# Performance work log

Hardware: AMD Instinct MI355X
Metric: run time of the kernel (lower is better)

Reference implementation:

```python
import jax, jax.numpy as jnp
import numpy as np

D_MODEL = 1024
NUM_MODULES = 8
MAX_TRANSLATION = 3.0
MAX_ROT_ANGLE = 3.141592653589793


def setup_inputs() -> dict:
    key = jax.random.key(0)
    k1, k2, k3, k4 = jax.random.split(key, 4)
    B, N = 8, 8192
    node_feats = jax.random.normal(k1, (B, N, D_MODEL), jnp.float32)
    coords = jax.random.normal(k2, (B, N, 3), jnp.float32)
    W = jax.random.normal(k3, (NUM_MODULES * 8, D_MODEL), jnp.float32) * (1.0 / np.sqrt(D_MODEL))
    b = jax.random.normal(k4, (NUM_MODULES * 8,), jnp.float32) * 0.01
    return {"node_feats": node_feats, "coords": coords, "W": W, "b": b}


def _normalize(x, eps=1e-12):
    return x / jnp.clip(jnp.linalg.norm(x, axis=-1, keepdims=True), eps)


def _axis_angle_to_quaternion(aa):
    # pytorch3d convention: quat = [cos(theta/2), axis * sin(theta/2)]
    angles = jnp.linalg.norm(aa, axis=-1, keepdims=True)
    half = angles * 0.5
    small = jnp.abs(angles) < 1e-6
    safe_angles = jnp.where(small, 1.0, angles)
    sin_half_over_angle = jnp.where(small, 0.5 - angles * angles / 48.0, jnp.sin(half) / safe_angles)
    return jnp.concatenate([jnp.cos(half), aa * sin_half_over_angle], axis=-1)


def _quat_mul(a, b):
    aw, ax, ay, az = a[..., 0], a[..., 1], a[..., 2], a[..., 3]
    bw, bx, by, bz = b[..., 0], b[..., 1], b[..., 2], b[..., 3]
    ow = aw * bw - ax * bx - ay * by - az * bz
    ox = aw * bx + ax * bw + ay * bz - az * by
    oy = aw * by - ax * bz + ay * bw + az * bx
    oz = aw * bz + ax * by - ay * bx + az * bw
    return jnp.stack([ow, ox, oy, oz], axis=-1)


def _quat_apply(q, p):
    # q: [B,1,4], p: [B,N,3] -> rotate points: im(q * (0,p) * q^-1)
    pq = jnp.concatenate([jnp.zeros_like(p[..., :1]), p], axis=-1)
    q_inv = q * jnp.array([1.0, -1.0, -1.0, -1.0], q.dtype)
    return _quat_mul(_quat_mul(q, pq), q_inv)[..., 1:]


def reference(node_feats, coords, W, b):
    B, N, _ = coords.shape
    params = (node_feats @ W.T + b).reshape(B, N, NUM_MODULES, 8)
    anchor_logits = params[..., 0:1]   # [B,N,M,1]
    select_logits = params[..., 1:2]
    rot_axis = params[..., 2:5]
    trans = params[..., 5:8]

    anchor_w = jax.nn.softmax(anchor_logits, axis=1)      # softmax over N
    select_p = jax.nn.sigmoid(select_logits)

    angles = jnp.linalg.norm(rot_axis, axis=-1, keepdims=True)
    axis_n = _normalize(rot_axis)
    angles = jnp.tanh(angles) * MAX_ROT_ANGLE
    quats = _axis_angle_to_quaternion(axis_n * angles)    # [B,N,M,4]
    trans = jnp.tanh(trans) * MAX_TRANSLATION             # [B,N,M,3]

    xs = (jnp.moveaxis(quats, 2, 0),     # [M,B,N,4]
          jnp.moveaxis(trans, 2, 0),     # [M,B,N,3]
          jnp.moveaxis(anchor_w, 2, 0),  # [M,B,N,1]
          jnp.moveaxis(select_p, 2, 0))  # [M,B,N,1]

    def step(c, per):
        q, t, aw, sp = per
        anchor = jnp.sum(c * aw, axis=1, keepdims=True)               # [B,1,3]
        s = jnp.clip(jnp.sum(sp, axis=1, keepdims=True), 1e-8)        # [B,1,1]
        q_group = _normalize(jnp.sum(q * sp, axis=1, keepdims=True) / s)  # [B,1,4]
        t_group = jnp.sum(t * sp, axis=1, keepdims=True) / s          # [B,1,3]
        moved = _quat_apply(q_group, c - anchor) + anchor + t_group   # [B,N,3]
        return c + sp * (moved - c), None                             # lerp

    out, _ = jax.lax.scan(step, coords, xs)
    return out
```

## Files before the change

kernel.cpp:

```cpp
#include <hip/hip_runtime.h>
#include <hip/hip_bf16.h>
#include <math.h>

#define D_MODEL 1024
#define NMOD 8
#define BATCH 8
#define NNODE 8192
#define PI_F 3.14159265358979323846f
#define MAXT 3.0f

typedef short bf16x8 __attribute__((ext_vector_type(8)));
typedef float f32x4 __attribute__((ext_vector_type(4)));

__device__ inline unsigned short f2bf(float x) {
    __hip_bfloat16 h = __float2bfloat16(x);
    return __builtin_bit_cast(unsigned short, h);
}
__device__ inline float bf2f(unsigned short h) {
    unsigned u = ((unsigned)h) << 16;
    return __builtin_bit_cast(float, u);
}

__global__ void pack_b(const float* __restrict__ W, unsigned short* __restrict__ Bpk) {
    int t = blockIdx.x * 256 + threadIdx.x;
    int l  = t & 63;
    int g  = (t >> 6) & 3;
    int ks = t >> 8;
    int j  = g * 16 + (l & 15);
    int k0 = ks * 32 + ((l >> 4) * 8);
    const float* wp = &W[(size_t)j * D_MODEL + k0];
    bf16x8 pack;
    #pragma unroll
    for (int r = 0; r < 8; ++r) pack[r] = (short)f2bf(wp[r]);
    *reinterpret_cast<bf16x8*>(Bpk + (size_t)t * 8) = pack;
}

__global__ __launch_bounds__(256, 4) void gemm_mfma(
    const float* __restrict__ feats, const unsigned short* __restrict__ Bpk,
    const float* __restrict__ bias,
    float* __restrict__ ew_out, float* __restrict__ sp_out,
    float* __restrict__ sums)
{
    __shared__ float pbuf[4][16][68];
    __shared__ float sacc[64];

    const int tid  = threadIdx.x;
    const int lane = tid & 63;
    const int wv   = tid >> 6;

    if (tid < 64) sacc[tid] = 0.f;
    __syncthreads();

    const int mt    = blockIdx.x * 4 + wv;
    const int mbase = mt * 16;
    const float* arow = feats + (size_t)(mbase + (lane & 15)) * D_MODEL + ((lane >> 4) * 8);
    const bf16x8* bp = reinterpret_cast<const bf16x8*>(Bpk);

    f32x4 acc[4];
    #pragma unroll
    for (int g = 0; g < 4; ++g) acc[g] = (f32x4){0.f, 0.f, 0.f, 0.f};

    #pragma unroll 2
    for (int ks = 0; ks < 32; ++ks) {
        const float4 fa = *reinterpret_cast<const float4*>(arow + ks * 32);
        const float4 fb = *reinterpret_cast<const float4*>(arow + ks * 32 + 4);
        float f[8] = {fa.x, fa.y, fa.z, fa.w, fb.x, fb.y, fb.z, fb.w};
        bf16x8 ahi, alo;
        #pragma unroll
        for (int i = 0; i < 8; ++i) {
            unsigned short h = f2bf(f[i]);
            ahi[i] = (short)h;
            alo[i] = (short)f2bf(f[i] - bf2f(h));
        }
        #pragma unroll
        for (int g = 0; g < 4; ++g) {
            bf16x8 bh = bp[(ks * 4 + g) * 64 + lane];
            acc[g] = __builtin_amdgcn_mfma_f32_16x16x32_bf16(ahi, bh, acc[g], 0, 0, 0);
            acc[g] = __builtin_amdgcn_mfma_f32_16x16x32_bf16(alo, bh, acc[g], 0, 0, 0);
        }
    }

    #pragma unroll
    for (int g = 0; g < 4; ++g) {
        float bj = bias[g * 16 + (lane & 15)];
        #pragma unroll
        for (int r = 0; r < 4; ++r)
            pbuf[wv][(lane >> 4) * 4 + r][g * 16 + (lane & 15)] = acc[g][r] + bj;
    }

    const int b    = mbase >> 13;
    const int nInB = mbase & 8191;

    #pragma unroll
    for (int h = 0; h < 2; ++h) {
        const int node = lane & 15;
        const int m    = (lane >> 4) + 4 * h;
        const float* pa = &pbuf[wv][node][m * 8];
        float al = pa[0], sl = pa[1];
        float ax = pa[2], ay = pa[3], az = pa[4];
        float tx = pa[5], ty = pa[6], tz = pa[7];

        float ew = expf(al);
        float sp = 1.f / (1.f + expf(-sl));

        float n0  = sqrtf(ax * ax + ay * ay + az * az);
        float inv = 1.f / fmaxf(n0, 1e-12f);
        float ang = tanhf(n0) * PI_F;
        float hf  = 0.5f * ang;
        float shoa = (ang < 1e-6f) ? (0.5f - ang * ang * (1.f / 48.f))
                                   : (sinf(hf) / ang);
        float qw = cosf(hf);
        float fac = inv * ang * shoa;
        float qx = ax * fac, qy = ay * fac, qz = az * fac;

        float ttx = tanhf(tx) * MAXT, tty = tanhf(ty) * MAXT, ttz = tanhf(tz) * MAXT;

        size_t base = ((size_t)(b * NMOD + m)) * NNODE + nInB + node;
        ew_out[base] = ew;
        sp_out[base] = sp;

        float red[8];
        red[0] = sp;
        red[1] = sp * qw; red[2] = sp * qx; red[3] = sp * qy; red[4] = sp * qz;
        red[5] = sp * ttx; red[6] = sp * tty; red[7] = sp * ttz;
        #pragma unroll
        for (int v = 0; v < 8; ++v) {
            #pragma unroll
            for (int o = 1; o < 16; o <<= 1) red[v] += __shfl_xor(red[v], o);
        }
        if ((lane & 15) == 0) {
            #pragma unroll
            for (int v = 0; v < 8; ++v) atomicAdd(&sacc[m * 8 + v], red[v]);
        }
    }
    __syncthreads();
    if (tid < 64) atomicAdd(&sums[b * 64 + tid], sacc[tid]);
}

__global__ __launch_bounds__(1024) void scan_coords(
    const float* __restrict__ coords,
    const float* __restrict__ ew_in, const float* __restrict__ sp_in,
    const float* __restrict__ sums, float* __restrict__ out)
{
    const int b   = blockIdx.x;
    const int tid = threadIdx.x;
    const int lane = tid & 63, wid = tid >> 6;
    __shared__ float redbuf[64];
    __shared__ float bcast[4];

    const int n0 = tid * 8;

    float cx[8], cy[8], cz[8];
    {
        float c[24];
        const float4* cp4 = reinterpret_cast<const float4*>(
            &coords[((size_t)b * NNODE + n0) * 3]);
        #pragma unroll
        for (int q = 0; q < 6; ++q) {
            float4 v = cp4[q];
            c[q * 4 + 0] = v.x; c[q * 4 + 1] = v.y;
            c[q * 4 + 2] = v.z; c[q * 4 + 3] = v.w;
        }
        #pragma unroll
        for (int i = 0; i < 8; ++i) { cx[i] = c[3*i]; cy[i] = c[3*i+1]; cz[i] = c[3*i+2]; }
    }

    for (int m = 0; m < NMOD; ++m) {
        const float* ewp = &ew_in[((size_t)b * NMOD + m) * NNODE];
        const float* spp = &sp_in[((size_t)b * NMOD + m) * NNODE];
        float ev[8], spl[8];
        {
            float4 e0 = *reinterpret_cast<const float4*>(&ewp[n0]);
            float4 e1 = *reinterpret_cast<const float4*>(&ewp[n0 + 4]);
            float4 s0 = *reinterpret_cast<const float4*>(&spp[n0]);
            float4 s1 = *reinterpret_cast<const float4*>(&spp[n0 + 4]);
            ev[0]=e0.x; ev[1]=e0.y; ev[2]=e0.z; ev[3]=e0.w;
            ev[4]=e1.x; ev[5]=e1.y; ev[6]=e1.z; ev[7]=e1.w;
            spl[0]=s0.x; spl[1]=s0.y; spl[2]=s0.z; spl[3]=s0.w;
            spl[4]=s1.x; spl[5]=s1.y; spl[6]=s1.z; spl[7]=s1.w;
        }
        float se = 0.f, sx = 0.f, sy = 0.f, sz = 0.f;
        #pragma unroll
        for (int i = 0; i < 8; ++i) {
            se += ev[i]; sx += ev[i] * cx[i]; sy += ev[i] * cy[i]; sz += ev[i] * cz[i];
        }
        float vals[4] = {se, sx, sy, sz};
        #pragma unroll
        for (int v = 0; v < 4; ++v) {
            float x = vals[v];
            #pragma unroll
            for (int o = 32; o > 0; o >>= 1) x += __shfl_down(x, o);
            if (lane == 0) redbuf[wid * 4 + v] = x;
        }
        __syncthreads();
        if (wid == 0) {
            float x = redbuf[lane];
            x += __shfl_down(x, 32);
            x += __shfl_down(x, 16);
            x += __shfl_down(x, 8);
            x += __shfl_down(x, 4);
            if (lane < 4) bcast[lane] = x;
        }
        __syncthreads();
        const float SE = bcast[0];
        const float AXc = bcast[1] / SE, AYc = bcast[2] / SE, AZc = bcast[3] / SE;

        const float* sm = &sums[((size_t)b * NMOD + m) * 8];
        float s  = fmaxf(sm[0], 1e-8f);
        float qw = sm[1] / s, qx = sm[2] / s, qy = sm[3] / s, qz = sm[4] / s;
        float qn = sqrtf(qw * qw + qx * qx + qy * qy + qz * qz);
        float qi = 1.f / fmaxf(qn, 1e-12f);
        qw *= qi; qx *= qi; qy *= qi; qz *= qi;
        float tgx = sm[5] / s, tgy = sm[6] / s, tgz = sm[7] / s;

        #pragma unroll
        for (int i = 0; i < 8; ++i) {
            float px = cx[i] - AXc, py = cy[i] - AYc, pz = cz[i] - AZc;
            float ux = qy * pz - qz * py;
            float uy = qz * px - qx * pz;
            float uz = qx * py - qy * px;
            float vx = qy * uz - qz * uy;
            float vy = qz * ux - qx * uz;
            float vz = qx * uy - qy * ux;
            float rx = px + 2.f * (qw * ux + vx);
            float ry = py + 2.f * (qw * uy + vy);
            float rz = pz + 2.f * (qw * uz + vz);
            float mx = rx + AXc + tgx, my = ry + AYc + tgy, mz = rz + AZc + tgz;
            float sp = spl[i];
            cx[i] += sp * (mx - cx[i]);
            cy[i] += sp * (my - cy[i]);
            cz[i] += sp * (mz - cz[i]);
        }
        __syncthreads();
    }

    {
        float c[24];
        #pragma unroll
        for (int i = 0; i < 8; ++i) { c[3*i] = cx[i]; c[3*i+1] = cy[i]; c[3*i+2] = cz[i]; }
        float4* op4 = reinterpret_cast<float4*>(&out[((size_t)b * NNODE + n0) * 3]);
        #pragma unroll
        for (int q = 0; q < 6; ++q)
            op4[q] = make_float4(c[q*4+0], c[q*4+1], c[q*4+2], c[q*4+3]);
    }
}

extern "C" void kernel_launch(void* const* d_in, const int* in_sizes, int n_in,
                              void* d_out, int out_size, void* d_ws, size_t ws_size,
                              hipStream_t stream) {
    const float* feats  = (const float*)d_in[0];
    const float* coords = (const float*)d_in[1];
    const float* W      = (const float*)d_in[2];
    const float* bias   = (const float*)d_in[3];
    float* out = (float*)d_out;

    char* ws = (char*)d_ws;
    unsigned short* Bpk = (unsigned short*)(ws);
    float* ew   = (float*)(ws + 262144);
    float* sp   = (float*)(ws + 262144 + 2097152);
    float* sums = (float*)(ws + 262144 + 2 * 2097152);

    hipMemsetAsync(sums, 0, (size_t)BATCH * NMOD * 8 * sizeof(float), stream);
    pack_b<<<32, 256, 0, stream>>>(W, Bpk);
    gemm_mfma<<<(BATCH * NNODE) / 64, 256, 0, stream>>>(feats, Bpk, bias, ew, sp, sums);
    scan_coords<<<BATCH, 1024, 0, stream>>>(coords, ew, sp, sums, out);
}
```

Baseline: 110.6 us.

## Use single bf16 MFMA pass, pack fp16 softmax/sigmoid weights, prefetch scan inputs

```diff
diff --git a/kernel.cpp b/kernel.cpp
--- a/kernel.cpp
+++ b/kernel.cpp
@@ -1,5 +1,6 @@
 #include <hip/hip_runtime.h>
 #include <hip/hip_bf16.h>
+#include <hip/hip_fp16.h>
 #include <math.h>
 
 #define D_MODEL 1024
@@ -16,9 +17,13 @@
     __hip_bfloat16 h = __float2bfloat16(x);
     return __builtin_bit_cast(unsigned short, h);
 }
-__device__ inline float bf2f(unsigned short h) {
-    unsigned u = ((unsigned)h) << 16;
-    return __builtin_bit_cast(float, u);
+__device__ inline float h2f(unsigned short u) {
+    __half h = __builtin_bit_cast(__half, u);
+    return __half2float(h);
+}
+__device__ inline unsigned short f2h(float x) {
+    __half h = __float2half(x);
+    return __builtin_bit_cast(unsigned short, h);
 }
 
 __global__ void pack_b(const float* __restrict__ W, unsigned short* __restrict__ Bpk) {
@@ -38,7 +43,7 @@
 __global__ __launch_bounds__(256, 4) void gemm_mfma(
     const float* __restrict__ feats, const unsigned short* __restrict__ Bpk,
     const float* __restrict__ bias,
-    float* __restrict__ ew_out, float* __restrict__ sp_out,
+    unsigned int* __restrict__ esp_out,
     float* __restrict__ sums)
 {
     __shared__ float pbuf[4][16][68];
@@ -65,18 +70,13 @@
         const float4 fa = *reinterpret_cast<const float4*>(arow + ks * 32);
         const float4 fb = *reinterpret_cast<const float4*>(arow + ks * 32 + 4);
         float f[8] = {fa.x, fa.y, fa.z, fa.w, fb.x, fb.y, fb.z, fb.w};
-        bf16x8 ahi, alo;
-        #pragma unroll
-        for (int i = 0; i < 8; ++i) {
-            unsigned short h = f2bf(f[i]);
-            ahi[i] = (short)h;
-            alo[i] = (short)f2bf(f[i] - bf2f(h));
-        }
+        bf16x8 a;
+        #pragma unroll
+        for (int i = 0; i < 8; ++i) a[i] = (short)f2bf(f[i]);
         #pragma unroll
         for (int g = 0; g < 4; ++g) {
             bf16x8 bh = bp[(ks * 4 + g) * 64 + lane];
-            acc[g] = __builtin_amdgcn_mfma_f32_16x16x32_bf16(ahi, bh, acc[g], 0, 0, 0);
-            acc[g] = __builtin_amdgcn_mfma_f32_16x16x32_bf16(alo, bh, acc[g], 0, 0, 0);
+            acc[g] = __builtin_amdgcn_mfma_f32_16x16x32_bf16(a, bh, acc[g], 0, 0, 0);
         }
     }
 
@@ -116,8 +116,7 @@
         float ttx = tanhf(tx) * MAXT, tty = tanhf(ty) * MAXT, ttz = tanhf(tz) * MAXT;
 
         size_t base = ((size_t)(b * NMOD + m)) * NNODE + nInB + node;
-        ew_out[base] = ew;
-        sp_out[base] = sp;
+        esp_out[base] = ((unsigned)f2h(sp) << 16) | (unsigned)f2h(ew);
 
         float red[8];
         red[0] = sp;
@@ -139,7 +138,7 @@
 
 __global__ __launch_bounds__(1024) void scan_coords(
     const float* __restrict__ coords,
-    const float* __restrict__ ew_in, const float* __restrict__ sp_in,
+    const unsigned int* __restrict__ esp_in,
     const float* __restrict__ sums, float* __restrict__ out)
 {
     const int b   = blockIdx.x;
@@ -165,20 +164,24 @@
         for (int i = 0; i < 8; ++i) { cx[i] = c[3*i]; cy[i] = c[3*i+1]; cz[i] = c[3*i+2]; }
     }
 
+    const uint4* esp4 = reinterpret_cast<const uint4*>(
+        &esp_in[(size_t)b * NMOD * NNODE]);
+    uint4 cur0 = esp4[(0 * NNODE + n0) >> 2];
+    uint4 cur1 = esp4[((0 * NNODE + n0) >> 2) + 1];
+
     for (int m = 0; m < NMOD; ++m) {
-        const float* ewp = &ew_in[((size_t)b * NMOD + m) * NNODE];
-        const float* spp = &sp_in[((size_t)b * NMOD + m) * NNODE];
+        const int mn = (m + 1 < NMOD) ? m + 1 : m;
+        uint4 nxt0 = esp4[(mn * NNODE + n0) >> 2];
+        uint4 nxt1 = esp4[((mn * NNODE + n0) >> 2) + 1];
+
+        unsigned pk[8] = {cur0.x, cur0.y, cur0.z, cur0.w, cur1.x, cur1.y, cur1.z, cur1.w};
         float ev[8], spl[8];
-        {
-            float4 e0 = *reinterpret_cast<const float4*>(&ewp[n0]);
-            float4 e1 = *reinterpret_cast<const float4*>(&ewp[n0 + 4]);
-            float4 s0 = *reinterpret_cast<const float4*>(&spp[n0]);
-            float4 s1 = *reinterpret_cast<const float4*>(&spp[n0 + 4]);
-            ev[0]=e0.x; ev[1]=e0.y; ev[2]=e0.z; ev[3]=e0.w;
-            ev[4]=e1.x; ev[5]=e1.y; ev[6]=e1.z; ev[7]=e1.w;
-            spl[0]=s0.x; spl[1]=s0.y; spl[2]=s0.z; spl[3]=s0.w;
-            spl[4]=s1.x; spl[5]=s1.y; spl[6]=s1.z; spl[7]=s1.w;
-        }
+        #pragma unroll
+        for (int i = 0; i < 8; ++i) {
+            ev[i]  = h2f((unsigned short)(pk[i] & 0xFFFFu));
+            spl[i] = h2f((unsigned short)(pk[i] >> 16));
+        }
+
         float se = 0.f, sx = 0.f, sy = 0.f, sz = 0.f;
         #pragma unroll
         for (int i = 0; i < 8; ++i) {
@@ -231,6 +234,7 @@
             cy[i] += sp * (my - cy[i]);
             cz[i] += sp * (mz - cz[i]);
         }
+        cur0 = nxt0; cur1 = nxt1;
         __syncthreads();
     }
 
@@ -256,12 +260,11 @@
 
     char* ws = (char*)d_ws;
     unsigned short* Bpk = (unsigned short*)(ws);
-    float* ew   = (float*)(ws + 262144);
-    float* sp   = (float*)(ws + 262144 + 2097152);
-    float* sums = (float*)(ws + 262144 + 2 * 2097152);
+    unsigned int* esp   = (unsigned int*)(ws + 262144);
+    float* sums         = (float*)(ws + 262144 + 2097152);
 
     hipMemsetAsync(sums, 0, (size_t)BATCH * NMOD * 8 * sizeof(float), stream);
     pack_b<<<32, 256, 0, stream>>>(W, Bpk);
-    gemm_mfma<<<(BATCH * NNODE) / 64, 256, 0, stream>>>(feats, Bpk, bias, ew, sp, sums);
-    scan_coords<<<BATCH, 1024, 0, stream>>>(coords, ew, sp, sums, out);
-}
+    gemm_mfma<<<(BATCH * NNODE) / 64, 256, 0, stream>>>(feats, Bpk, bias, esp, sums);
+    scan_coords<<<BATCH, 1024, 0, stream>>>(coords, esp, sums, out);
+}
```

Measured after the change: 104.6 us. 1.06x faster.
